# Optimization experiments

Measured on AMD Instinct MI355X. Metric: run time of the kernel, lower is better.

## Reference

```python
import jax, jax.numpy as jnp
import numpy as np

BLOCK = 64      # base classifier input height/width
STRIDE = 16     # BLOCK // 4 per Windowing(stride=[1,bh/4,bw/4,1], size=[1,bh,bw,1])
K = 10          # n_classes
THRESH = 0.7    # bbox_threshold


def extract_patches(x):
    # x: [B,H,W,C] -> [B,R,Cc,BLOCK*BLOCK*C], same layout as tf.image.extract_patches
    B, H, Wd, C = x.shape
    R = (H - BLOCK) // STRIDE + 1
    Cc = (Wd - BLOCK) // STRIDE + 1
    rows = jnp.arange(R)[:, None] * STRIDE + jnp.arange(BLOCK)[None, :]   # [R,64]
    cols = jnp.arange(Cc)[:, None] * STRIDE + jnp.arange(BLOCK)[None, :]  # [Cc,64]
    p = x[:, rows]                 # [B,R,64,W,C]
    p = p[:, :, :, cols]           # [B,R,64,Cc,64,C]
    p = jnp.transpose(p, (0, 1, 3, 2, 4, 5))  # [B,R,Cc,64,64,C]
    return p.reshape(B, R, Cc, BLOCK * BLOCK * C)


def connected_components(mask):
    # 4-connected components of a 2D bool mask via iterative min-label propagation.
    # Background = 0; foreground labels are distinct positive ints per component.
    R, C = mask.shape
    big = jnp.int32(R * C + 2)
    init = jnp.where(mask, jnp.arange(1, R * C + 1, dtype=jnp.int32).reshape(R, C), 0)

    def step(lab, _):
        l = jnp.where(mask, lab, big)
        up = jnp.concatenate([jnp.full((1, C), big, l.dtype), l[:-1]], 0)
        dn = jnp.concatenate([l[1:], jnp.full((1, C), big, l.dtype)], 0)
        lf = jnp.concatenate([jnp.full((R, 1), big, l.dtype), l[:, :-1]], 1)
        rt = jnp.concatenate([l[:, 1:], jnp.full((R, 1), big, l.dtype)], 1)
        m = jnp.minimum(jnp.minimum(l, jnp.minimum(up, dn)), jnp.minimum(lf, rt))
        return jnp.where(mask, m, 0), None

    lab, _ = jax.lax.scan(step, init, None, length=2 * (R + C))
    return lab


def boxes_from_labels(lab):
    # Segmented min/max over label ids replaces the per-region python loop:
    # box = [rowmin-1, colmin-1, rowmax+1, colmax+1] per component.
    R, C = lab.shape
    N = R * C
    flat = lab.reshape(N)
    rr = jnp.arange(N, dtype=jnp.int32) // C
    cc = jnp.arange(N, dtype=jnp.int32) % C
    rmin = jax.ops.segment_min(rr, flat, num_segments=N + 1)
    cmin = jax.ops.segment_min(cc, flat, num_segments=N + 1)
    rmax = jax.ops.segment_max(rr, flat, num_segments=N + 1)
    cmax = jax.ops.segment_max(cc, flat, num_segments=N + 1)
    cnt = jax.ops.segment_sum(jnp.ones(N, jnp.int32), flat, num_segments=N + 1)
    valid = (cnt > 0).at[0].set(False)  # slot 0 is background
    boxes = jnp.stack([rmin - 1, cmin - 1, rmax + 1, cmax + 1], -1)
    boxes = jnp.where(valid[:, None], boxes, 0)
    return boxes, valid


def setup_inputs() -> dict:
    key = jax.random.key(0)
    k1, k2, k3 = jax.random.split(key, 3)
    inputs = jax.random.normal(k1, (1, 1024, 1024, 3), dtype=jnp.float32)
    # scale W so logits have ~unit variance -> sparse (realistic) threshold mask
    W = jax.random.normal(k2, (12288, K), dtype=jnp.float32) * 0.01
    b = jax.random.normal(k3, (K,), dtype=jnp.float32)
    return {"inputs": inputs, "W": W, "b": b}


def reference(inputs, W, b):
    patches = extract_patches(inputs)               # [1,R,Cc,D]
    B, R, Cc, D = patches.shape
    logits = patches.reshape(B * R * Cc, D) @ W + b # [N,K]
    prob = jax.nn.softmax(logits, axis=1).reshape(R, Cc, K)
    mask = prob > THRESH                            # [R,Cc,K]
    labels = jax.vmap(connected_components, in_axes=2, out_axes=2)(mask)  # [R,Cc,K]
    boxes, valid = jax.vmap(boxes_from_labels)(jnp.transpose(labels, (2, 0, 1)))
    # boxes: [K, R*Cc+1, 4] padded per-component bboxes; valid: [K, R*Cc+1]
    return prob, labels, boxes, valid
```

## Files before the change

### kernel.cpp

```cpp
#include <hip/hip_runtime.h>
#include <cmath>

#define RR 61
#define NCELL 3721
#define KCLS 10
#define DDIM 12288
#define BIGV 0x0FFFFFFF
#define PITCH 64

#define OUT_PROB 0
#define OUT_LAB  37210
#define OUT_BOX  74420
#define OUT_VALID 223300

__global__ __launch_bounds__(1024) void k1_logits(
    const float* __restrict__ x, const float* __restrict__ W,
    const float* __restrict__ b, float* __restrict__ out)
{
    const int tid  = threadIdx.x;
    const int tsub = tid & 255;
    const int wrow = tid >> 8;
    const int blk  = blockIdx.x;
    const int rg   = blk >> 4;
    const int cg   = blk & 15;

    int r = rg * 4 + wrow; if (r > 60) r = 60;
    const int c0 = cg * 4;

    float acc[4][KCLS];
#pragma unroll
    for (int p = 0; p < 4; ++p)
#pragma unroll
        for (int k = 0; k < KCLS; ++k) acc[p][k] = 0.0f;

    int coff[4];
#pragma unroll
    for (int p = 0; p < 4; ++p) {
        int c = c0 + p; if (c > 60) c = 60;
        coff[p] = c * 48;
    }
    const int rbase = r * 49152;

    int i   = (tsub >= 192) ? 1 : 0;
    int rem = tsub - i * 192;

#pragma unroll 2
    for (int it = 0; it < 48; ++it) {
        const int d = tsub + (it << 8);
        const float* xp = x + rbase + i * 3072 + rem;
        float xv[4];
#pragma unroll
        for (int p = 0; p < 4; ++p) xv[p] = xp[coff[p]];

        const float2* wp = (const float2*)(W + (size_t)d * KCLS);
        const float2 w0 = wp[0], w1 = wp[1], w2 = wp[2], w3 = wp[3], w4 = wp[4];
        const float wv[KCLS] = { w0.x, w0.y, w1.x, w1.y, w2.x, w2.y,
                                 w3.x, w3.y, w4.x, w4.y };
#pragma unroll
        for (int p = 0; p < 4; ++p)
#pragma unroll
            for (int k = 0; k < KCLS; ++k) acc[p][k] += xv[p] * wv[k];

        rem += 64; ++i;
        if (rem >= 192) { rem -= 192; ++i; }
    }

#pragma unroll
    for (int p = 0; p < 4; ++p)
#pragma unroll
        for (int k = 0; k < KCLS; ++k) {
            float v = acc[p][k];
#pragma unroll
            for (int off = 32; off > 0; off >>= 1) v += __shfl_down(v, off);
            acc[p][k] = v;
        }

    __shared__ float red[4][4][4][KCLS];
    const int wgrp = (tsub >> 6);
    if ((tsub & 63) == 0) {
#pragma unroll
        for (int p = 0; p < 4; ++p)
#pragma unroll
            for (int k = 0; k < KCLS; ++k) red[wrow][wgrp][p][k] = acc[p][k];
    }
    __syncthreads();

    if (tid < 16) {
        const int wr = tid >> 2;
        const int p  = tid & 3;
        const int rr = rg * 4 + wr;
        const int cc = c0 + p;
        if (rr <= 60 && cc <= 60) {
            double l[KCLS];
#pragma unroll
            for (int k = 0; k < KCLS; ++k)
                l[k] = (double)red[wr][0][p][k] + (double)red[wr][1][p][k]
                     + (double)red[wr][2][p][k] + (double)red[wr][3][p][k]
                     + (double)b[k];
            double m = l[0];
#pragma unroll
            for (int k = 1; k < KCLS; ++k) m = fmax(m, l[k]);
            double e[KCLS], s = 0.0;
#pragma unroll
            for (int k = 0; k < KCLS; ++k) { e[k] = exp(l[k] - m); s += e[k]; }
            const double inv = 1.0 / s;
            float* po = out + OUT_PROB + (size_t)(rr * 61 + cc) * KCLS;
#pragma unroll
            for (int k = 0; k < KCLS; ++k) po[k] = (float)(e[k] * inv);
        }
    }
}

__global__ __launch_bounds__(1024) void k2_cc_boxes(float* __restrict__ out)
{
    const int k   = blockIdx.x;
    const int tid = threadIdx.x;

    __shared__ int lab[63 * PITCH];
    __shared__ int act[NCELL];
    __shared__ int nact;
    __shared__ int changed;
    __shared__ int rmn[NCELL + 1], rmx[NCELL + 1], cmn[NCELL + 1], cmx[NCELL + 1];

    for (int idx = tid; idx < 63 * PITCH; idx += 1024) lab[idx] = BIGV;
    for (int s = tid; s <= NCELL; s += 1024) {
        rmn[s] = 0x7fffffff; cmn[s] = 0x7fffffff; rmx[s] = -1; cmx[s] = -1;
    }
    if (tid == 0) nact = 0;
    __syncthreads();

    for (int idx = tid; idx < NCELL; idx += 1024) {
        const float pv = out[OUT_PROB + (size_t)idx * KCLS + k];
        if (pv > 0.7f) {
            const int r = idx / 61, c = idx - r * 61;
            const int off = (r + 1) * PITCH + (c + 1);
            lab[off] = idx + 1;
            act[atomicAdd(&nact, 1)] = off;
        }
    }
    __syncthreads();
    const int na = nact;

    for (int iter = 0; iter < 600; ++iter) {
        if (tid == 0) changed = 0;
        __syncthreads();
        bool ch = false;
        for (int idx = tid; idx < na; idx += 1024) {
            const int off = act[idx];
            int v = lab[off];
            int t;
            t = lab[off - 1];     if (t < v) v = t;
            t = lab[off + 1];     if (t < v) v = t;
            t = lab[off - PITCH]; if (t < v) v = t;
            t = lab[off + PITCH]; if (t < v) v = t;
            if (v < lab[off]) { lab[off] = v; ch = true; }
        }
        if (ch) changed = 1;
        __syncthreads();
        if (changed == 0) break;
        __syncthreads();
    }

    for (int idx = tid; idx < na; idx += 1024) {
        const int off = act[idx];
        const int lb  = lab[off];
        const int r = (off >> 6) - 1, c = (off & 63) - 1;
        atomicMin(&rmn[lb], r); atomicMax(&rmx[lb], r);
        atomicMin(&cmn[lb], c); atomicMax(&cmx[lb], c);
    }
    __syncthreads();

    for (int idx = tid; idx < NCELL; idx += 1024) {
        const int r = idx / 61, c = idx - r * 61;
        const int v = lab[(r + 1) * PITCH + (c + 1)];
        out[OUT_LAB + (size_t)idx * KCLS + k] = (float)((v < BIGV) ? v : 0);
    }
    for (int s = tid; s <= NCELL; s += 1024) {
        const bool val = (s > 0) && (rmx[s] >= 0);
        float* bo = out + OUT_BOX + (size_t)(k * (NCELL + 1) + s) * 4;
        if (val) {
            bo[0] = (float)(rmn[s] - 1);
            bo[1] = (float)(cmn[s] - 1);
            bo[2] = (float)(rmx[s] + 1);
            bo[3] = (float)(cmx[s] + 1);
        } else {
            bo[0] = 0.0f; bo[1] = 0.0f; bo[2] = 0.0f; bo[3] = 0.0f;
        }
        out[OUT_VALID + (size_t)k * (NCELL + 1) + s] = val ? 1.0f : 0.0f;
    }
}

extern "C" void kernel_launch(void* const* d_in, const int* in_sizes, int n_in,
                              void* d_out, int out_size, void* d_ws, size_t ws_size,
                              hipStream_t stream) {
    const float* x = (const float*)d_in[0];
    const float* W = (const float*)d_in[1];
    const float* b = (const float*)d_in[2];
    float* out = (float*)d_out;

    k1_logits  <<<dim3(256), dim3(1024), 0, stream>>>(x, W, b, out);
    k2_cc_boxes<<<dim3(KCLS), dim3(1024), 0, stream>>>(out);
}
```

Before: 105.2 us.

## Stage W in swizzled LDS, widen column tiles, DPP reductions, pointer-jumping CC

The logits kernel now stages W chunks into double-buffered, bank-swizzled shared memory with register prefetch. Each block covers 2 rows × 8 columns with the D dimension split across thread groups, which cuts redundant global W reads. Wave reductions use DPP instead of shuffles. The connected-components kernel switches to offset-based labels with pointer-jumping (union-find style atomicMin), which should converge in far fewer rounds; it caps iterations at 128 and remaps labels to cell indices on output. This adds more LDS pressure and syncs per iteration, and the iteration cap risks non-convergence on unusual masks.

```diff
diff --git a/kernel.cpp b/kernel.cpp
--- a/kernel.cpp
+++ b/kernel.cpp
@@ -1,17 +1,34 @@
 #include <hip/hip_runtime.h>
 #include <cmath>
 
-#define RR 61
+#define KCLS 10
 #define NCELL 3721
-#define KCLS 10
-#define DDIM 12288
-#define BIGV 0x0FFFFFFF
-#define PITCH 64
+#define BIGV  0x0FFFFFFF
 
 #define OUT_PROB 0
 #define OUT_LAB  37210
 #define OUT_BOX  74420
 #define OUT_VALID 223300
+
+#define DPPADD(x, ctrl) \
+    x += __int_as_float(__builtin_amdgcn_update_dpp( \
+        0, __float_as_int(x), ctrl, 0xf, 0xf, true))
+
+__device__ __forceinline__ float wave_sum64(float x) {
+    DPPADD(x, 0x111);
+    DPPADD(x, 0x112);
+    DPPADD(x, 0x114);
+    DPPADD(x, 0x118);
+    DPPADD(x, 0x142);
+    DPPADD(x, 0x143);
+    return x;
+}
+
+__device__ __forceinline__ int swz_fidx(int j) {
+    const int row = j / 10;
+    const int c   = j - row * 10;
+    return (row << 4) + (((c >> 2) ^ ((row >> 1) & 3)) << 2) + (c & 3);
+}
 
 __global__ __launch_bounds__(1024) void k1_logits(
     const float* __restrict__ x, const float* __restrict__ W,
@@ -19,91 +36,125 @@
 {
     const int tid  = threadIdx.x;
     const int tsub = tid & 255;
-    const int wrow = tid >> 8;
+    const int g    = tid >> 8;
+    const int wrow = g & 1;
+    const int dsl  = g >> 1;
     const int blk  = blockIdx.x;
-    const int rg   = blk >> 4;
-    const int cg   = blk & 15;
-
-    int r = rg * 4 + wrow; if (r > 60) r = 60;
-    const int c0 = cg * 4;
-
-    float acc[4][KCLS];
-#pragma unroll
-    for (int p = 0; p < 4; ++p)
+    const int rg   = blk >> 3;
+    const int cg   = blk & 7;
+
+    int r = rg * 2 + wrow; if (r > 60) r = 60;
+    const int c0 = (cg == 7) ? 53 : cg * 8;
+
+    __shared__ float  wbuf[2][512 * 16];
+    __shared__ float  red[2][2][4][8][KCLS];
+    __shared__ double lgs[16][KCLS];
+
+    const int j0 = tid << 2;
+    const int d0 = swz_fidx(j0);
+    const int d1 = swz_fidx(j0 + 2);
+    const int d2 = swz_fidx(4096 + tid);
+
+    const int row = tsub + (dsl << 8);
+    const int s3  = (row >> 1) & 3;
+    const int rb  = row << 4;
+    const int wo0 = rb + ((0 ^ s3) << 2);
+    const int wo1 = rb + ((1 ^ s3) << 2);
+    const int wo2 = rb + ((2 ^ s3) << 2);
+
+    int i   = row / 192;
+    int rem = row - i * 192;
+    const float* xb = x + r * 49152 + c0 * 48;
+
+    float acc[8][KCLS];
+#pragma unroll
+    for (int p = 0; p < 8; ++p)
 #pragma unroll
         for (int k = 0; k < KCLS; ++k) acc[p][k] = 0.0f;
 
-    int coff[4];
-#pragma unroll
-    for (int p = 0; p < 4; ++p) {
-        int c = c0 + p; if (c > 60) c = 60;
-        coff[p] = c * 48;
-    }
-    const int rbase = r * 49152;
-
-    int i   = (tsub >= 192) ? 1 : 0;
-    int rem = tsub - i * 192;
-
-#pragma unroll 2
-    for (int it = 0; it < 48; ++it) {
-        const int d = tsub + (it << 8);
-        const float* xp = x + rbase + i * 3072 + rem;
-        float xv[4];
-#pragma unroll
-        for (int p = 0; p < 4; ++p) xv[p] = xp[coff[p]];
-
-        const float2* wp = (const float2*)(W + (size_t)d * KCLS);
-        const float2 w0 = wp[0], w1 = wp[1], w2 = wp[2], w3 = wp[3], w4 = wp[4];
-        const float wv[KCLS] = { w0.x, w0.y, w1.x, w1.y, w2.x, w2.y,
-                                 w3.x, w3.y, w4.x, w4.y };
-#pragma unroll
-        for (int p = 0; p < 4; ++p)
+    float4 sv; float s1;
+    {
+        const float4 v0 = *(const float4*)(W + j0);
+        const float  v1 = W[4096 + tid];
+        float* wb0 = &wbuf[0][0];
+        *(float2*)(wb0 + d0) = make_float2(v0.x, v0.y);
+        *(float2*)(wb0 + d1) = make_float2(v0.z, v0.w);
+        wb0[d2] = v1;
+        const float* ws = W + 5120;
+        sv = *(const float4*)(ws + j0);
+        s1 = ws[4096 + tid];
+    }
+
+    for (int it = 0; it < 24; ++it) {
+        __syncthreads();
+        if (it + 1 < 24) {
+            float* wbn = &wbuf[(it + 1) & 1][0];
+            *(float2*)(wbn + d0) = make_float2(sv.x, sv.y);
+            *(float2*)(wbn + d1) = make_float2(sv.z, sv.w);
+            wbn[d2] = s1;
+            if (it + 2 < 24) {
+                const float* ws = W + (it + 2) * 5120;
+                sv = *(const float4*)(ws + j0);
+                s1 = ws[4096 + tid];
+            }
+        }
+        const float* wb = &wbuf[it & 1][0];
+        const float4 wa  = *(const float4*)(wb + wo0);
+        const float4 wbq = *(const float4*)(wb + wo1);
+        const float2 wc  = *(const float2*)(wb + wo2);
+        const float wv[KCLS] = { wa.x, wa.y, wa.z, wa.w,
+                                 wbq.x, wbq.y, wbq.z, wbq.w, wc.x, wc.y };
+        const float* xp = xb + i * 3072 + rem;
+        float xv[8];
+#pragma unroll
+        for (int p = 0; p < 8; ++p) xv[p] = xp[p * 48];
+#pragma unroll
+        for (int p = 0; p < 8; ++p)
 #pragma unroll
             for (int k = 0; k < KCLS; ++k) acc[p][k] += xv[p] * wv[k];
 
-        rem += 64; ++i;
+        rem += 128; i += 2;
         if (rem >= 192) { rem -= 192; ++i; }
     }
 
-#pragma unroll
-    for (int p = 0; p < 4; ++p)
+    const int w4 = tsub >> 6;
+#pragma unroll
+    for (int p = 0; p < 8; ++p)
 #pragma unroll
         for (int k = 0; k < KCLS; ++k) {
-            float v = acc[p][k];
-#pragma unroll
-            for (int off = 32; off > 0; off >>= 1) v += __shfl_down(v, off);
-            acc[p][k] = v;
-        }
-
-    __shared__ float red[4][4][4][KCLS];
-    const int wgrp = (tsub >> 6);
-    if ((tsub & 63) == 0) {
-#pragma unroll
-        for (int p = 0; p < 4; ++p)
-#pragma unroll
-            for (int k = 0; k < KCLS; ++k) red[wrow][wgrp][p][k] = acc[p][k];
+            const float s = wave_sum64(acc[p][k]);
+            if ((tid & 63) == 63) red[wrow][dsl][w4][p][k] = s;
+        }
+    __syncthreads();
+
+    if (tid < 160) {
+        const int wr  = tid / 80;
+        const int t80 = tid - wr * 80;
+        const int p   = t80 / 10;
+        const int kk  = t80 - p * 10;
+        double s = (double)b[kk];
+#pragma unroll
+        for (int ds = 0; ds < 2; ++ds)
+#pragma unroll
+            for (int w = 0; w < 4; ++w) s += (double)red[wr][ds][w][p][kk];
+        lgs[wr * 8 + p][kk] = s;
     }
     __syncthreads();
 
     if (tid < 16) {
-        const int wr = tid >> 2;
-        const int p  = tid & 3;
-        const int rr = rg * 4 + wr;
-        const int cc = c0 + p;
-        if (rr <= 60 && cc <= 60) {
+        const int wr = tid >> 3, p = tid & 7;
+        const int rr = rg * 2 + wr, cc = c0 + p;
+        if (rr <= 60) {
             double l[KCLS];
 #pragma unroll
-            for (int k = 0; k < KCLS; ++k)
-                l[k] = (double)red[wr][0][p][k] + (double)red[wr][1][p][k]
-                     + (double)red[wr][2][p][k] + (double)red[wr][3][p][k]
-                     + (double)b[k];
+            for (int k = 0; k < KCLS; ++k) l[k] = lgs[tid][k];
             double m = l[0];
 #pragma unroll
             for (int k = 1; k < KCLS; ++k) m = fmax(m, l[k]);
-            double e[KCLS], s = 0.0;
-#pragma unroll
-            for (int k = 0; k < KCLS; ++k) { e[k] = exp(l[k] - m); s += e[k]; }
-            const double inv = 1.0 / s;
+            double e[KCLS], ssum = 0.0;
+#pragma unroll
+            for (int k = 0; k < KCLS; ++k) { e[k] = exp(l[k] - m); ssum += e[k]; }
+            const double inv = 1.0 / ssum;
             float* po = out + OUT_PROB + (size_t)(rr * 61 + cc) * KCLS;
 #pragma unroll
             for (int k = 0; k < KCLS; ++k) po[k] = (float)(e[k] * inv);
@@ -116,13 +167,12 @@
     const int k   = blockIdx.x;
     const int tid = threadIdx.x;
 
-    __shared__ int lab[63 * PITCH];
+    __shared__ int lab[63 * 64];
     __shared__ int act[NCELL];
-    __shared__ int nact;
-    __shared__ int changed;
+    __shared__ int nact, changed;
     __shared__ int rmn[NCELL + 1], rmx[NCELL + 1], cmn[NCELL + 1], cmx[NCELL + 1];
 
-    for (int idx = tid; idx < 63 * PITCH; idx += 1024) lab[idx] = BIGV;
+    for (int idx = tid; idx < 63 * 64; idx += 1024) lab[idx] = BIGV;
     for (int s = tid; s <= NCELL; s += 1024) {
         rmn[s] = 0x7fffffff; cmn[s] = 0x7fffffff; rmx[s] = -1; cmx[s] = -1;
     }
@@ -133,27 +183,33 @@
         const float pv = out[OUT_PROB + (size_t)idx * KCLS + k];
         if (pv > 0.7f) {
             const int r = idx / 61, c = idx - r * 61;
-            const int off = (r + 1) * PITCH + (c + 1);
-            lab[off] = idx + 1;
+            const int off = (r + 1) * 64 + (c + 1);
+            lab[off] = off;
             act[atomicAdd(&nact, 1)] = off;
         }
     }
     __syncthreads();
     const int na = nact;
 
-    for (int iter = 0; iter < 600; ++iter) {
+    for (int round = 0; round < 128; ++round) {
         if (tid == 0) changed = 0;
         __syncthreads();
         bool ch = false;
-        for (int idx = tid; idx < na; idx += 1024) {
-            const int off = act[idx];
-            int v = lab[off];
-            int t;
-            t = lab[off - 1];     if (t < v) v = t;
-            t = lab[off + 1];     if (t < v) v = t;
-            t = lab[off - PITCH]; if (t < v) v = t;
-            t = lab[off + PITCH]; if (t < v) v = t;
-            if (v < lab[off]) { lab[off] = v; ch = true; }
+        for (int ii = tid; ii < na; ii += 1024) {
+            const int off = act[ii];
+            const int v = lab[off];
+            int m = v, t;
+            t = lab[off - 1];  if (t < m) m = t;
+            t = lab[off + 1];  if (t < m) m = t;
+            t = lab[off - 64]; if (t < m) m = t;
+            t = lab[off + 64]; if (t < m) m = t;
+            if (m < v) {
+                int p = lab[m];
+                while (p < m) { m = p; p = lab[m]; }
+                atomicMin(&lab[off], m);
+                atomicMin(&lab[v],   m);
+                ch = true;
+            }
         }
         if (ch) changed = 1;
         __syncthreads();
@@ -161,20 +217,23 @@
         __syncthreads();
     }
 
-    for (int idx = tid; idx < na; idx += 1024) {
-        const int off = act[idx];
-        const int lb  = lab[off];
+    for (int idx = tid; idx < NCELL; idx += 1024) {
+        const int r = idx / 61, c = idx - r * 61;
+        const int v = lab[(r + 1) * 64 + (c + 1)];
+        const int lv = (v < BIGV) ? ((v >> 6) * 61 - 61 + (v & 63)) : 0;
+        out[OUT_LAB + (size_t)idx * KCLS + k] = (float)lv;
+    }
+
+    for (int ii = tid; ii < na; ii += 1024) {
+        const int off = act[ii];
+        const int v = lab[off];
+        const int lb = (v >> 6) * 61 - 61 + (v & 63);
         const int r = (off >> 6) - 1, c = (off & 63) - 1;
         atomicMin(&rmn[lb], r); atomicMax(&rmx[lb], r);
         atomicMin(&cmn[lb], c); atomicMax(&cmx[lb], c);
     }
     __syncthreads();
 
-    for (int idx = tid; idx < NCELL; idx += 1024) {
-        const int r = idx / 61, c = idx - r * 61;
-        const int v = lab[(r + 1) * PITCH + (c + 1)];
-        out[OUT_LAB + (size_t)idx * KCLS + k] = (float)((v < BIGV) ? v : 0);
-    }
     for (int s = tid; s <= NCELL; s += 1024) {
         const bool val = (s > 0) && (rmx[s] >= 0);
         float* bo = out + OUT_BOX + (size_t)(k * (NCELL + 1) + s) * 4;
@@ -198,6 +257,6 @@
     const float* b = (const float*)d_in[2];
     float* out = (float*)d_out;
 
-    k1_logits  <<<dim3(256), dim3(1024), 0, stream>>>(x, W, b, out);
+    k1_logits  <<<dim3(248), dim3(1024), 0, stream>>>(x, W, b, out);
     k2_cc_boxes<<<dim3(KCLS), dim3(1024), 0, stream>>>(out);
 }
```

New measurement: 91.95 us. 12.6% less time.
